# Performance work log

Hardware: AMD Instinct MI355X
Metric: run time of the kernel (lower is better)

The kernel has to match this reference:

```python
import jax, jax.numpy as jnp
import numpy as np

N, IN_DIM, D, H, L, E, MAX_DEG = 50000, 128, 128, 16, 3, 800000, 512
C = D // H  # head dim


def _ln(x, scale, bias, eps=1e-5):
    mu = x.mean(-1, keepdims=True)
    var = ((x - mu) ** 2).mean(-1, keepdims=True)
    return (x - mu) * jax.lax.rsqrt(var + eps) * scale + bias


def setup_inputs() -> dict:
    key = jax.random.key(0)
    ks = jax.random.split(key, 20)
    s = 0.02
    inp = {
        "x": jax.random.normal(ks[0], (N, IN_DIM), jnp.float32),
        "edge_index": jax.random.randint(ks[1], (2, E), 0, N, jnp.int32),
        "W_in": jax.random.normal(ks[2], (IN_DIM, D), jnp.float32) * s,
        "b_in": jnp.zeros((D,), jnp.float32),
        "in_emb": jax.random.normal(ks[3], (MAX_DEG + 1, D), jnp.float32) * s,
        "out_emb": jax.random.normal(ks[4], (MAX_DEG + 1, D), jnp.float32) * s,
        "ln_scale": jnp.ones((L, D), jnp.float32),
        "ln_bias": jnp.zeros((L, D), jnp.float32),
        "Wq": jax.random.normal(ks[5], (L, D, D), jnp.float32) * s,
        "bq": jnp.zeros((L, D), jnp.float32),
        "Wk": jax.random.normal(ks[6], (L, D, D), jnp.float32) * s,
        "bk": jnp.zeros((L, D), jnp.float32),
        "Wv": jax.random.normal(ks[7], (L, D, D), jnp.float32) * s,
        "bv": jnp.zeros((L, D), jnp.float32),
        "Wskip": jax.random.normal(ks[8], (L, D, D), jnp.float32) * s,
        "bskip": jnp.zeros((L, D), jnp.float32),
        "Wbeta": jax.random.normal(ks[9], (L, 3 * D, 1), jnp.float32) * s,
        "fn_scale": jnp.ones((D,), jnp.float32),
        "fn_bias": jnp.zeros((D,), jnp.float32),
    }
    return inp


def _transformer_conv(h, src, tgt, Wq, bq, Wk, bk, Wv, bv, Wskip, bskip, Wbeta):
    # PyG TransformerConv, beta=True, concat=True, eval mode (no dropout)
    q = (h @ Wq + bq).reshape(N, H, C)
    k = (h @ Wk + bk).reshape(N, H, C)
    v = (h @ Wv + bv).reshape(N, H, C)
    # per-edge attention logits [E, H]
    alpha = (q[tgt] * k[src]).sum(-1) / jnp.sqrt(jnp.float32(C))
    # scatter-softmax over incoming edges of each target node
    m = jax.ops.segment_max(alpha, tgt, num_segments=N)
    ex = jnp.exp(alpha - m[tgt])
    den = jax.ops.segment_sum(ex, tgt, num_segments=N)
    w = ex / den[tgt]  # [E, H]
    msg = v[src] * w[:, :, None]  # [E, H, C]
    out = jax.ops.segment_sum(msg, tgt, num_segments=N).reshape(N, D)
    # root skip + gated beta combination
    xr = h @ Wskip + bskip
    beta = jax.nn.sigmoid(jnp.concatenate([out, xr, out - xr], axis=-1) @ Wbeta)
    return beta * xr + (1.0 - beta) * out


def reference(x, edge_index, W_in, b_in, in_emb, out_emb, ln_scale, ln_bias,
              Wq, bq, Wk, bk, Wv, bv, Wskip, bskip, Wbeta, fn_scale, fn_bias):
    src, tgt = edge_index[0], edge_index[1]
    h = x @ W_in + b_in
    # centrality encoding: in/out degree embeddings
    ones = jnp.ones((E,), jnp.float32)
    idg = jnp.clip(jax.ops.segment_sum(ones, tgt, num_segments=N), 0, MAX_DEG).astype(jnp.int32)
    odg = jnp.clip(jax.ops.segment_sum(ones, src, num_segments=N), 0, MAX_DEG).astype(jnp.int32)
    h = h + in_emb[idg] + out_emb[odg]
    for l in range(L):
        hn = _ln(h, ln_scale[l], ln_bias[l])
        h = h + _transformer_conv(hn, src, tgt, Wq[l], bq[l], Wk[l], bk[l],
                                  Wv[l], bv[l], Wskip[l], bskip[l], Wbeta[l])
    return _ln(h, fn_scale, fn_bias)
```

## Files before the change

kernel.cpp:

```cpp
#include <hip/hip_runtime.h>
#include <math.h>
#include <stdint.h>

#define NN 50000
#define DM 128
#define NH 16
#define HC 8
#define NL 3
#define NE 800000
#define MAXDEG 512
#define NRG 1563

#define NB2 782
#define NBLK 256
#define CNTN (NB2 * NBLK)
#define SC1 196
#define RNG 4
#define REP 16

typedef __attribute__((ext_vector_type(8))) short short8;
typedef __attribute__((ext_vector_type(4))) float f32x4;
typedef __attribute__((ext_vector_type(2))) float f32x2;

static __device__ __forceinline__ unsigned short f2bf(float x) {
    union { float f; unsigned int u; } v; v.f = x;
    unsigned int r = (v.u + 0x7fffu + ((v.u >> 16) & 1u)) >> 16;
    return (unsigned short)r;
}
static __device__ __forceinline__ float bf2f(unsigned short b) {
    union { unsigned int u; float f; } v; v.u = ((unsigned int)b) << 16;
    return v.f;
}

__global__ __launch_bounds__(1024) void hist_out_kernel(const int* __restrict__ ei,
                                                        unsigned int* __restrict__ part) {
    __shared__ unsigned int hp[8192];
    int rg = blockIdx.x;
    int rp = blockIdx.y;
    int t = threadIdx.x;
    for (int i = t; i < 8192; i += 1024) hp[i] = 0;
    __syncthreads();
    int lo = rg << 14;
    for (int e = rp * 1024 + t; e < NE; e += REP * 1024) {
        int s = ei[e] - lo;
        if ((unsigned)s < 16384u)
            atomicAdd(&hp[s >> 1], (s & 1) ? 0x10000u : 1u);
    }
    __syncthreads();
    unsigned int* pp = part + (size_t)(rg * REP + rp) * 8192;
    for (int i = t; i < 8192; i += 1024) pp[i] = hp[i];
}
__global__ __launch_bounds__(256) void hist_reduce_kernel(const unsigned int* __restrict__ part,
                                                          int* __restrict__ outdeg) {
    int wd = blockIdx.x * 256 + threadIdx.x;
    if (wd >= 25000) return;
    int rg = wd >> 13, lw = wd & 8191;
    unsigned int sum = 0;
#pragma unroll
    for (int r = 0; r < REP; r++)
        sum += part[(size_t)(rg * REP + r) * 8192 + lw];
    outdeg[2 * wd] = sum & 0xffff;
    if (2 * wd + 1 < NN) outdeg[2 * wd + 1] = sum >> 16;
}

__global__ __launch_bounds__(256) void p1_count_kernel(const int* __restrict__ ei,
                                                       int* __restrict__ cnt) {
    __shared__ int hh[NB2];
    int t = threadIdx.x, blk = blockIdx.x;
    for (int b = t; b < NB2; b += 256) hh[b] = 0;
    __syncthreads();
    for (int e = blk * 256 + t; e < NE; e += NBLK * 256)
        atomicAdd(&hh[ei[NE + e] >> 6], 1);
    __syncthreads();
    for (int b = t; b < NB2; b += 256) cnt[b * NBLK + blk] = hh[b];
}

__global__ __launch_bounds__(1024) void gscan1_kernel(int* __restrict__ data,
                                                      int* __restrict__ bsum, int n) {
    __shared__ int sd[1024];
    int t = threadIdx.x;
    int i = blockIdx.x * 1024 + t;
    int val = (i < n) ? data[i] : 0;
    sd[t] = val;
    __syncthreads();
    for (int d = 1; d < 1024; d <<= 1) {
        int x = (t >= d) ? sd[t - d] : 0;
        __syncthreads();
        sd[t] += x;
        __syncthreads();
    }
    if (i < n) data[i] = sd[t] - val;
    if (t == 1023) bsum[blockIdx.x] = sd[1023];
}
__global__ void gscan2_kernel(const int* __restrict__ bsum, int* __restrict__ bpre, int nb) {
    int run = 0;
    for (int i = 0; i < nb; i++) { bpre[i] = run; run += bsum[i]; }
}
__global__ __launch_bounds__(1024) void gscan3_kernel(int* __restrict__ data,
                                                      const int* __restrict__ bpre, int n) {
    int i = blockIdx.x * 1024 + threadIdx.x;
    if (i < n) data[i] += bpre[blockIdx.x];
}

__global__ __launch_bounds__(256) void p3_scatter_kernel(const int* __restrict__ ei,
                                                         const int* __restrict__ cnt,
                                                         int* __restrict__ tmp) {
    __shared__ int hh[NB2];
    int t = threadIdx.x, blk = blockIdx.x;
    for (int b = t; b < NB2; b += 256) hh[b] = cnt[b * NBLK + blk];
    __syncthreads();
    for (int e = blk * 256 + t; e < NE; e += NBLK * 256) {
        int s = ei[e], tg = ei[NE + e];
        int pos = atomicAdd(&hh[tg >> 6], 1);
        tmp[pos] = ((tg & 63) << 16) | s;
    }
}

__global__ __launch_bounds__(256) void p4_fine_kernel(const int* __restrict__ tmp,
                                                      const int* __restrict__ cnt,
                                                      int* __restrict__ off,
                                                      int* __restrict__ indeg,
                                                      int* __restrict__ srcs) {
    __shared__ int c64[64], x64[64], cur[64];
    int b = blockIdx.x, t = threadIdx.x;
    int e0 = cnt[b * NBLK];
    int e1 = (b == NB2 - 1) ? NE : cnt[(b + 1) * NBLK];
    if (t < 64) c64[t] = 0;
    __syncthreads();
    for (int i = e0 + t; i < e1; i += 256) atomicAdd(&c64[(tmp[i] >> 16) & 63], 1);
    __syncthreads();
    if (t == 0) {
        int run = 0;
        for (int j = 0; j < 64; j++) { x64[j] = run; cur[j] = e0 + run; run += c64[j]; }
    }
    __syncthreads();
    if (t < 64) {
        int node = b * 64 + t;
        if (node <= NN) off[node] = e0 + x64[t];
        if (node < NN) indeg[node] = c64[t];
    }
    __syncthreads();
    for (int i = e0 + t; i < e1; i += 256) {
        int w = tmp[i];
        int pos = atomicAdd(&cur[(w >> 16) & 63], 1);
        srcs[pos] = w & 0xffff;
    }
}

__global__ __launch_bounds__(256) void wprep_kernel(const float* __restrict__ Wq,
                                                    const float* __restrict__ Wk,
                                                    const float* __restrict__ Wv,
                                                    const float* __restrict__ Ws,
                                                    const float* __restrict__ Win,
                                                    unsigned short* __restrict__ Wt) {
    __shared__ unsigned short lds[128 * 130];
    int bid = blockIdx.x;
    const float* W;
    if (bid == 12) {
        W = Win;
    } else {
        int l = bid >> 2, m = bid & 3;
        W = (m == 0 ? Wq : m == 1 ? Wk : m == 2 ? Wv : Ws) + (size_t)l * DM * DM;
    }
    unsigned short* out = Wt + (size_t)bid * DM * DM;
    int t = threadIdx.x;
    for (int i = t; i < DM * DM; i += 256) {
        int kk = i >> 7, c = i & 127;
        lds[kk * 130 + c] = f2bf(W[i]);
    }
    __syncthreads();
    for (int o = t; o < DM * DM; o += 256) {
        int c = o >> 7, kk = o & 127;
        out[o] = lds[kk * 130 + c];
    }
}

__global__ __launch_bounds__(256) void xcast_kernel(const float* __restrict__ x,
                                                    unsigned short* __restrict__ xb) {
    int i = blockIdx.x * 256 + threadIdx.x;
    float4 xv = ((const float4*)x)[i];
    ushort4 o;
    o.x = f2bf(xv.x); o.y = f2bf(xv.y); o.z = f2bf(xv.z); o.w = f2bf(xv.w);
    ((ushort4*)xb)[i] = o;
}

__global__ __launch_bounds__(256) void gemm_in_mfma(const unsigned short* __restrict__ xb,
                                                    const unsigned short* __restrict__ Wt,
                                                    const float* __restrict__ b,
                                                    const float* __restrict__ in_emb,
                                                    const float* __restrict__ out_emb,
                                                    const int* __restrict__ indeg,
                                                    const int* __restrict__ outdeg,
                                                    float* __restrict__ h) {
    int w = threadIdx.x >> 6;
    int l = threadIdx.x & 63;
    int lr = l & 15, lc = l >> 4;
    int colbase = (w & 1) * 64;
    int rhalf = w >> 1;

    short8 bfrag[4][4];
#pragma unroll
    for (int ct = 0; ct < 4; ct++) {
        const unsigned short* bp = Wt + (size_t)(colbase + ct * 16 + lr) * DM;
#pragma unroll
        for (int kk = 0; kk < 4; kk++)
            bfrag[ct][kk] = *(const short8*)(bp + kk * 32 + lc * 8);
    }

    for (int rg = blockIdx.x * 2 + rhalf; rg < NRG; rg += gridDim.x * 2) {
        int n0 = rg * 32;
        short8 afrag[2][4];
#pragma unroll
        for (int rt = 0; rt < 2; rt++) {
            int row = n0 + rt * 16 + lr;
            if (row >= NN) row = NN - 1;
            const unsigned short* ap = xb + (size_t)row * DM;
#pragma unroll
            for (int kk = 0; kk < 4; kk++)
                afrag[rt][kk] = *(const short8*)(ap + kk * 32 + lc * 8);
        }
        f32x4 acc[2][4];
#pragma unroll
        for (int rt = 0; rt < 2; rt++)
#pragma unroll
            for (int ct = 0; ct < 4; ct++)
                acc[rt][ct] = (f32x4){0.f, 0.f, 0.f, 0.f};
#pragma unroll
        for (int kk = 0; kk < 4; kk++)
#pragma unroll
            for (int rt = 0; rt < 2; rt++)
#pragma unroll
                for (int ct = 0; ct < 4; ct++)
                    acc[rt][ct] = __builtin_amdgcn_mfma_f32_16x16x32_bf16(
                        afrag[rt][kk], bfrag[ct][kk], acc[rt][ct], 0, 0, 0);
#pragma unroll
        for (int rt = 0; rt < 2; rt++) {
#pragma unroll
            for (int j = 0; j < 4; j++) {
                int row = n0 + rt * 16 + lc * 4 + j;
                if (row < NN) {
                    int id = min(indeg[row], MAXDEG);
                    int od = min(outdeg[row], MAXDEG);
#pragma unroll
                    for (int ct = 0; ct < 4; ct++) {
                        int cc = colbase + ct * 16 + lr;
                        h[(size_t)row * DM + cc] = acc[rt][ct][j] + b[cc]
                            + in_emb[id * DM + cc] + out_emb[od * DM + cc];
                    }
                }
            }
        }
    }
}

static __device__ __forceinline__ void ln_body(const float* __restrict__ hp,
                                               const float* __restrict__ sc,
                                               const float* __restrict__ bi,
                                               int lane, float* o0, float* o1) {
    float v0 = hp[lane], v1 = hp[lane + 64];
    float s = v0 + v1;
#pragma unroll
    for (int d = 32; d; d >>= 1) s += __shfl_xor(s, d);
    float mu = s * (1.f / 128.f);
    float d0 = v0 - mu, d1 = v1 - mu;
    float vs = d0 * d0 + d1 * d1;
#pragma unroll
    for (int d = 32; d; d >>= 1) vs += __shfl_xor(vs, d);
    float rstd = rsqrtf(vs * (1.f / 128.f) + 1e-5f);
    *o0 = d0 * rstd * sc[lane] + bi[lane];
    *o1 = d1 * rstd * sc[lane + 64] + bi[lane + 64];
}

__global__ __launch_bounds__(256) void ln_bf16_kernel(const float* __restrict__ h,
                                                      const float* __restrict__ sc,
                                                      const float* __restrict__ bi,
                                                      unsigned short* __restrict__ o) {
    int row = blockIdx.x * 4 + (threadIdx.x >> 6);
    int lane = threadIdx.x & 63;
    float a, b;
    ln_body(h + (size_t)row * DM, sc, bi, lane, &a, &b);
    unsigned short* op = o + (size_t)row * DM;
    op[lane] = f2bf(a);
    op[lane + 64] = f2bf(b);
}

__global__ __launch_bounds__(256) void ln_f32_kernel(const float* __restrict__ h,
                                                     const float* __restrict__ sc,
                                                     const float* __restrict__ bi,
                                                     float* __restrict__ o) {
    int row = blockIdx.x * 4 + (threadIdx.x >> 6);
    int lane = threadIdx.x & 63;
    float a, b;
    ln_body(h + (size_t)row * DM, sc, bi, lane, &a, &b);
    float* op = o + (size_t)row * DM;
    op[lane] = a;
    op[lane + 64] = b;
}

__global__ __launch_bounds__(512) void gemm_qkvs_mfma(const unsigned short* __restrict__ hn,
                                                      const unsigned short* __restrict__ Wt,
                                                      const float* __restrict__ bq, const float* __restrict__ bk,
                                                      const float* __restrict__ bv, const float* __restrict__ bs,
                                                      unsigned short* __restrict__ q,
                                                      unsigned char* __restrict__ kv8,
                                                      unsigned short* __restrict__ xrb) {
    int w = threadIdx.x >> 6;
    int l = threadIdx.x & 63;
    int lr = l & 15, lc = l >> 4;
    int colbase = w * 64;
    int m = w >> 1;
    int cmbase = (w & 1) * 64;

    const float* bptr = (m == 0 ? bq : m == 1 ? bk : m == 2 ? bv : bs);
    short8 bfrag[4][4];
    float biasv[4];
#pragma unroll
    for (int ct = 0; ct < 4; ct++) {
        int col = colbase + ct * 16 + lr;
        const unsigned short* bp = Wt + (size_t)col * DM;
#pragma unroll
        for (int kk = 0; kk < 4; kk++)
            bfrag[ct][kk] = *(const short8*)(bp + kk * 32 + lc * 8);
        biasv[ct] = bptr[cmbase + ct * 16 + lr];
    }

    for (int rg = blockIdx.x; rg < NRG; rg += gridDim.x) {
        int n0 = rg * 32;
        short8 afrag[2][4];
#pragma unroll
        for (int rt = 0; rt < 2; rt++) {
            int row = n0 + rt * 16 + lr;
            if (row >= NN) row = NN - 1;
            const unsigned short* ap = hn + (size_t)row * DM;
#pragma unroll
            for (int kk = 0; kk < 4; kk++)
                afrag[rt][kk] = *(const short8*)(ap + kk * 32 + lc * 8);
        }
        f32x4 acc[2][4];
#pragma unroll
        for (int rt = 0; rt < 2; rt++)
#pragma unroll
            for (int ct = 0; ct < 4; ct++)
                acc[rt][ct] = (f32x4){0.f, 0.f, 0.f, 0.f};
#pragma unroll
        for (int kk = 0; kk < 4; kk++)
#pragma unroll
            for (int rt = 0; rt < 2; rt++)
#pragma unroll
                for (int ct = 0; ct < 4; ct++)
                    acc[rt][ct] = __builtin_amdgcn_mfma_f32_16x16x32_bf16(
                        afrag[rt][kk], bfrag[ct][kk], acc[rt][ct], 0, 0, 0);

        if (m == 0 || m == 3) {
            unsigned short* dst = (m == 0) ? q : xrb;
#pragma unroll
            for (int rt = 0; rt < 2; rt++)
#pragma unroll
                for (int ct = 0; ct < 4; ct++) {
                    int cc = cmbase + ct * 16 + lr;
                    float bb = biasv[ct];
#pragma unroll
                    for (int j = 0; j < 4; j++) {
                        int row = n0 + rt * 16 + lc * 4 + j;
                        if (row < NN) dst[(size_t)row * DM + cc] = f2bf(acc[rt][ct][j] + bb);
                    }
                }
        } else {
            unsigned char* base = kv8 + ((m == 1) ? 0 : 4);
#pragma unroll
            for (int rt = 0; rt < 2; rt++)
#pragma unroll
                for (int ct = 0; ct < 4; ct++) {
                    int cc = cmbase + ct * 16 + lr;
                    int goff = (cc >> 2) * 8;
                    float bb = biasv[ct];
#pragma unroll
                    for (int j = 0; j < 4; j++) {
                        float val = acc[rt][ct][j] + bb;
                        float nb = __shfl_xor(val, 1);
                        float a = (lr & 1) ? nb : val;
                        float b2 = (lr & 1) ? val : nb;
                        int w2 = __builtin_amdgcn_cvt_pk_fp8_f32(a, b2, 0, false);
                        int p = __shfl_xor(w2, 2);
                        unsigned int word = (lr & 2)
                            ? ((unsigned int)(p & 0xffff) | ((unsigned int)w2 << 16))
                            : ((unsigned int)(w2 & 0xffff) | ((unsigned int)p << 16));
                        int row = n0 + rt * 16 + lc * 4 + j;
                        if ((lr & 3) == 0 && row < NN)
                            *(unsigned int*)(base + (size_t)row * 256 + goff) = word;
                    }
                }
        }
    }
}

__global__ __launch_bounds__(256) void attn_fused_kernel(const int* __restrict__ off,
                                                         const int* __restrict__ srcs,
                                                         const unsigned short* __restrict__ q,
                                                         const unsigned char* __restrict__ kv8,
                                                         const unsigned short* __restrict__ xrb,
                                                         const float* __restrict__ Wb,
                                                         float* __restrict__ h,
                                                         const float* __restrict__ nsc,
                                                         const float* __restrict__ nbi,
                                                         unsigned short* __restrict__ hn_out) {
    int wv = threadIdx.x >> 6;
    int L = threadIdx.x & 63;
    int half = L >> 5, L5 = L & 31;
    int n = blockIdx.x * 4 + wv;
    int o0 = off[n], o1 = off[n + 1];
    int c4 = L5 * 4;
    const float isq = 0.35355339059f;

    ushort4 qu = *(const ushort4*)(q + (size_t)n * DM + c4);
    float q0 = bf2f(qu.x) * isq, q1 = bf2f(qu.y) * isq,
          q2 = bf2f(qu.z) * isq, q3 = bf2f(qu.w) * isq;

    float den = 0.f, a0 = 0.f, a1 = 0.f, a2 = 0.f, a3 = 0.f;
    for (int p = o0; p < o1; p += 16) {
        int sj[8];
#pragma unroll
        for (int j = 0; j < 8; j++) {
            int e = p + 2 * j + half;
            sj[j] = (e < o1) ? srcs[e] : 0;
        }
        uint2 uu[8];
#pragma unroll
        for (int j = 0; j < 8; j++)
            uu[j] = *(const uint2*)(kv8 + (size_t)sj[j] * 256 + L5 * 8);
#pragma unroll
        for (int j = 0; j < 8; j++) {
            int e = p + 2 * j + half;
            f32x2 k01 = __builtin_amdgcn_cvt_pk_f32_fp8(uu[j].x, false);
            f32x2 k23 = __builtin_amdgcn_cvt_pk_f32_fp8(uu[j].x, true);
            f32x2 v01 = __builtin_amdgcn_cvt_pk_f32_fp8(uu[j].y, false);
            f32x2 v23 = __builtin_amdgcn_cvt_pk_f32_fp8(uu[j].y, true);
            float d = q0 * k01.x + q1 * k01.y + q2 * k23.x + q3 * k23.y;
            d += __shfl_xor(d, 1);
            float e2 = (e < o1) ? __expf(d) : 0.f;
            den += e2;
            a0 += e2 * v01.x;
            a1 += e2 * v01.y;
            a2 += e2 * v23.x;
            a3 += e2 * v23.y;
        }
    }
    den += __shfl_xor(den, 32);
    a0 += __shfl_xor(a0, 32);
    a1 += __shfl_xor(a1, 32);
    a2 += __shfl_xor(a2, 32);
    a3 += __shfl_xor(a3, 32);

    float inv = (den > 0.f) ? 1.f / den : 0.f;
    float o0v = a0 * inv, o1v = a1 * inv, o2v = a2 * inv, o3v = a3 * inv;

    ushort4 xu = *(const ushort4*)(xrb + (size_t)n * DM + c4);
    float x0 = bf2f(xu.x), x1 = bf2f(xu.y), x2 = bf2f(xu.z), x3 = bf2f(xu.w);
    float c = o0v * Wb[c4] + o1v * Wb[c4 + 1] + o2v * Wb[c4 + 2] + o3v * Wb[c4 + 3]
            + x0 * Wb[DM + c4] + x1 * Wb[DM + c4 + 1]
            + x2 * Wb[DM + c4 + 2] + x3 * Wb[DM + c4 + 3]
            + (o0v - x0) * Wb[2 * DM + c4] + (o1v - x1) * Wb[2 * DM + c4 + 1]
            + (o2v - x2) * Wb[2 * DM + c4 + 2] + (o3v - x3) * Wb[2 * DM + c4 + 3];
    if (half) c = 0.f;
#pragma unroll
    for (int d2 = 32; d2; d2 >>= 1) c += __shfl_xor(c, d2);
    float beta = 1.f / (1.f + __expf(-c));

    size_t idx = (size_t)n * DM + c4;
    float4 hv = *(const float4*)(h + idx);
    hv.x += beta * x0 + (1.f - beta) * o0v;
    hv.y += beta * x1 + (1.f - beta) * o1v;
    hv.z += beta * x2 + (1.f - beta) * o2v;
    hv.w += beta * x3 + (1.f - beta) * o3v;
    if (half == 0) *(float4*)(h + idx) = hv;

    if (hn_out) {
        float s = hv.x + hv.y + hv.z + hv.w;
#pragma unroll
        for (int d2 = 16; d2; d2 >>= 1) s += __shfl_xor(s, d2);
        float mu = s * (1.f / 128.f);
        float d0 = hv.x - mu, d1 = hv.y - mu, d2_ = hv.z - mu, d3 = hv.w - mu;
        float vs = d0 * d0 + d1 * d1 + d2_ * d2_ + d3 * d3;
#pragma unroll
        for (int d2 = 16; d2; d2 >>= 1) vs += __shfl_xor(vs, d2);
        float rstd = rsqrtf(vs * (1.f / 128.f) + 1e-5f);
        float4 scv = *(const float4*)(nsc + c4);
        float4 biv = *(const float4*)(nbi + c4);
        ushort4 o;
        o.x = f2bf(d0 * rstd * scv.x + biv.x);
        o.y = f2bf(d1 * rstd * scv.y + biv.y);
        o.z = f2bf(d2_ * rstd * scv.z + biv.z);
        o.w = f2bf(d3 * rstd * scv.w + biv.w);
        if (half == 0) *(ushort4*)(hn_out + idx) = o;
    }
}

static inline char* alignup(char* p) {
    return (char*)(((uintptr_t)p + 255) & ~(uintptr_t)255);
}

extern "C" void kernel_launch(void* const* d_in, const int* in_sizes, int n_in,
                              void* d_out, int out_size, void* d_ws, size_t ws_size,
                              hipStream_t stream) {
    const float* x       = (const float*)d_in[0];
    const int*   ei      = (const int*)d_in[1];
    const float* W_in    = (const float*)d_in[2];
    const float* b_in    = (const float*)d_in[3];
    const float* in_emb  = (const float*)d_in[4];
    const float* out_emb = (const float*)d_in[5];
    const float* ln_sc   = (const float*)d_in[6];
    const float* ln_bi   = (const float*)d_in[7];
    const float* Wq      = (const float*)d_in[8];
    const float* bq      = (const float*)d_in[9];
    const float* Wk      = (const float*)d_in[10];
    const float* bk      = (const float*)d_in[11];
    const float* Wv      = (const float*)d_in[12];
    const float* bv      = (const float*)d_in[13];
    const float* Wsk     = (const float*)d_in[14];
    const float* bsk     = (const float*)d_in[15];
    const float* Wbeta   = (const float*)d_in[16];
    const float* fn_sc   = (const float*)d_in[17];
    const float* fn_bi   = (const float*)d_in[18];

    char* w = (char*)d_ws;
    int* indeg  = (int*)w; w = alignup(w + (size_t)NN * 4);
    int* outdeg = (int*)w; w = alignup(w + (size_t)NN * 4);
    int* off    = (int*)w; w = alignup(w + (size_t)(NN + 1) * 4);
    int* srcs   = (int*)w; w = alignup(w + (size_t)NE * 4);
    int* tmp    = (int*)w; w = alignup(w + (size_t)NE * 4);
    int* cnt    = (int*)w; w = alignup(w + (size_t)CNTN * 4);
    int* bsum   = (int*)w; w = alignup(w + (size_t)SC1 * 4);
    int* bpre   = (int*)w; w = alignup(w + (size_t)SC1 * 4);
    unsigned int* hpart = (unsigned int*)w; w = alignup(w + (size_t)RNG * REP * 8192 * 4);
    float* h    = (float*)w; w = alignup(w + (size_t)NN * DM * 4);
    unsigned short* hn  = (unsigned short*)w; w = alignup(w + (size_t)NN * DM * 2);
    unsigned short* q   = (unsigned short*)w; w = alignup(w + (size_t)NN * DM * 2);
    unsigned short* xrb = (unsigned short*)w; w = alignup(w + (size_t)NN * DM * 2);
    unsigned char*  kv8 = (unsigned char*)w;  w = alignup(w + (size_t)NN * 256);
    unsigned short* xb  = (unsigned short*)w; w = alignup(w + (size_t)NN * DM * 2);
    unsigned short* Wt  = (unsigned short*)w; w = alignup(w + (size_t)13 * DM * DM * 2);

    hist_out_kernel<<<dim3(RNG, REP), 1024, 0, stream>>>(ei, hpart);
    hist_reduce_kernel<<<98, 256, 0, stream>>>(hpart, outdeg);
    p1_count_kernel<<<NBLK, 256, 0, stream>>>(ei, cnt);
    gscan1_kernel<<<SC1, 1024, 0, stream>>>(cnt, bsum, CNTN);
    gscan2_kernel<<<1, 1, 0, stream>>>(bsum, bpre, SC1);
    gscan3_kernel<<<SC1, 1024, 0, stream>>>(cnt, bpre, CNTN);
    p3_scatter_kernel<<<NBLK, 256, 0, stream>>>(ei, cnt, tmp);
    p4_fine_kernel<<<NB2, 256, 0, stream>>>(tmp, cnt, off, indeg, srcs);

    wprep_kernel<<<13, 256, 0, stream>>>(Wq, Wk, Wv, Wsk, W_in, Wt);
    xcast_kernel<<<NN * DM / 4 / 256, 256, 0, stream>>>(x, xb);

    gemm_in_mfma<<<391, 256, 0, stream>>>(xb, Wt + (size_t)12 * DM * DM, b_in,
                                          in_emb, out_emb, indeg, outdeg, h);
    ln_bf16_kernel<<<NN / 4, 256, 0, stream>>>(h, ln_sc, ln_bi, hn);
    for (int l = 0; l < NL; l++) {
        gemm_qkvs_mfma<<<391, 512, 0, stream>>>(hn,
            Wt + (size_t)l * 4 * DM * DM,
            bq + l * DM, bk + l * DM, bv + l * DM, bsk + l * DM,
            q, kv8, xrb);
        bool last = (l == NL - 1);
        attn_fused_kernel<<<NN / 4, 256, 0, stream>>>(off, srcs, q, kv8, xrb,
            Wbeta + (size_t)l * 3 * DM, h,
            last ? (const float*)nullptr : ln_sc + (l + 1) * DM,
            last ? (const float*)nullptr : ln_bi + (l + 1) * DM,
            last ? (unsigned short*)nullptr : hn);
    }
    ln_f32_kernel<<<NN / 4, 256, 0, stream>>>(h, fn_sc, fn_bi, (float*)d_out);
}
```

Measured before the change: 387.8 us.

## Stage QKV/skip GEMM outputs through swizzled LDS for coalesced vector stores

The QKV+skip GEMM writes its bias-added bf16 results into a swizzled shared-memory tile instead of scattering 2-byte stores straight from MFMA fragments. After a barrier, each thread writes 16-byte coalesced rows of q and xr, and packs k/v into interleaved fp8 words. The grid now launches one block per 32-row group instead of a persistent loop, so weight fragments are reloaded per block. k and v are rounded to bf16 before the fp8 conversion, which adds a double rounding step.

```diff
diff --git a/kernel.cpp b/kernel.cpp
--- a/kernel.cpp
+++ b/kernel.cpp
@@ -304,6 +304,8 @@
                                                       unsigned short* __restrict__ q,
                                                       unsigned char* __restrict__ kv8,
                                                       unsigned short* __restrict__ xrb) {
+    __shared__ unsigned short qlds[8 * 2048];
+
     int w = threadIdx.x >> 6;
     int l = threadIdx.x & 63;
     int lr = l & 15, lc = l >> 4;
@@ -324,73 +326,82 @@
         biasv[ct] = bptr[cmbase + ct * 16 + lr];
     }
 
-    for (int rg = blockIdx.x; rg < NRG; rg += gridDim.x) {
-        int n0 = rg * 32;
-        short8 afrag[2][4];
-#pragma unroll
-        for (int rt = 0; rt < 2; rt++) {
-            int row = n0 + rt * 16 + lr;
-            if (row >= NN) row = NN - 1;
-            const unsigned short* ap = hn + (size_t)row * DM;
-#pragma unroll
-            for (int kk = 0; kk < 4; kk++)
-                afrag[rt][kk] = *(const short8*)(ap + kk * 32 + lc * 8);
+    int n0 = blockIdx.x * 32;
+    short8 afrag[2][4];
+#pragma unroll
+    for (int rt = 0; rt < 2; rt++) {
+        int row = n0 + rt * 16 + lr;
+        if (row >= NN) row = NN - 1;
+        const unsigned short* ap = hn + (size_t)row * DM;
+#pragma unroll
+        for (int kk = 0; kk < 4; kk++)
+            afrag[rt][kk] = *(const short8*)(ap + kk * 32 + lc * 8);
+    }
+    f32x4 acc[2][4];
+#pragma unroll
+    for (int rt = 0; rt < 2; rt++)
+#pragma unroll
+        for (int ct = 0; ct < 4; ct++)
+            acc[rt][ct] = (f32x4){0.f, 0.f, 0.f, 0.f};
+#pragma unroll
+    for (int kk = 0; kk < 4; kk++)
+#pragma unroll
+        for (int rt = 0; rt < 2; rt++)
+#pragma unroll
+            for (int ct = 0; ct < 4; ct++)
+                acc[rt][ct] = __builtin_amdgcn_mfma_f32_16x16x32_bf16(
+                    afrag[rt][kk], bfrag[ct][kk], acc[rt][ct], 0, 0, 0);
+
+    unsigned short* tile = qlds + w * 2048;
+#pragma unroll
+    for (int rt = 0; rt < 2; rt++)
+#pragma unroll
+        for (int ct = 0; ct < 4; ct++) {
+            float bb = biasv[ct];
+            int grp = ct ^ lc;
+#pragma unroll
+            for (int j = 0; j < 4; j++) {
+                int rloc = rt * 16 + lc * 4 + j;
+                tile[rloc * 64 + grp * 16 + lr] = f2bf(acc[rt][ct][j] + bb);
+            }
         }
-        f32x4 acc[2][4];
-#pragma unroll
-        for (int rt = 0; rt < 2; rt++)
-#pragma unroll
-            for (int ct = 0; ct < 4; ct++)
-                acc[rt][ct] = (f32x4){0.f, 0.f, 0.f, 0.f};
-#pragma unroll
-        for (int kk = 0; kk < 4; kk++)
-#pragma unroll
-            for (int rt = 0; rt < 2; rt++)
-#pragma unroll
-                for (int ct = 0; ct < 4; ct++)
-                    acc[rt][ct] = __builtin_amdgcn_mfma_f32_16x16x32_bf16(
-                        afrag[rt][kk], bfrag[ct][kk], acc[rt][ct], 0, 0, 0);
-
-        if (m == 0 || m == 3) {
-            unsigned short* dst = (m == 0) ? q : xrb;
-#pragma unroll
-            for (int rt = 0; rt < 2; rt++)
-#pragma unroll
-                for (int ct = 0; ct < 4; ct++) {
-                    int cc = cmbase + ct * 16 + lr;
-                    float bb = biasv[ct];
-#pragma unroll
-                    for (int j = 0; j < 4; j++) {
-                        int row = n0 + rt * 16 + lc * 4 + j;
-                        if (row < NN) dst[(size_t)row * DM + cc] = f2bf(acc[rt][ct][j] + bb);
-                    }
-                }
-        } else {
-            unsigned char* base = kv8 + ((m == 1) ? 0 : 4);
-#pragma unroll
-            for (int rt = 0; rt < 2; rt++)
-#pragma unroll
-                for (int ct = 0; ct < 4; ct++) {
-                    int cc = cmbase + ct * 16 + lr;
-                    int goff = (cc >> 2) * 8;
-                    float bb = biasv[ct];
-#pragma unroll
-                    for (int j = 0; j < 4; j++) {
-                        float val = acc[rt][ct][j] + bb;
-                        float nb = __shfl_xor(val, 1);
-                        float a = (lr & 1) ? nb : val;
-                        float b2 = (lr & 1) ? val : nb;
-                        int w2 = __builtin_amdgcn_cvt_pk_fp8_f32(a, b2, 0, false);
-                        int p = __shfl_xor(w2, 2);
-                        unsigned int word = (lr & 2)
-                            ? ((unsigned int)(p & 0xffff) | ((unsigned int)w2 << 16))
-                            : ((unsigned int)(w2 & 0xffff) | ((unsigned int)p << 16));
-                        int row = n0 + rt * 16 + lc * 4 + j;
-                        if ((lr & 3) == 0 && row < NN)
-                            *(unsigned int*)(base + (size_t)row * 256 + goff) = word;
-                    }
-                }
+    __syncthreads();
+
+    int t5 = threadIdx.x;
+    int r = t5 >> 4;
+    int g = t5 & 15;
+    int row = n0 + r;
+    if (row < NN) {
+        int c0 = g * 8;
+        int c0L = c0 & 63;
+        int sw = (r >> 2) & 3;
+        int loff = r * 64 + (((c0L >> 4) ^ sw) << 4) + (c0L & 15);
+        int hi = c0 >> 6;
+
+        short8 vq = *(const short8*)(qlds + (0 * 2 + hi) * 2048 + loff);
+        *(short8*)(q + (size_t)row * DM + c0) = vq;
+        short8 vx = *(const short8*)(qlds + (3 * 2 + hi) * 2048 + loff);
+        *(short8*)(xrb + (size_t)row * DM + c0) = vx;
+        short8 vk = *(const short8*)(qlds + (1 * 2 + hi) * 2048 + loff);
+        short8 vv = *(const short8*)(qlds + (2 * 2 + hi) * 2048 + loff);
+        float kf[8], vf[8];
+#pragma unroll
+        for (int i = 0; i < 8; i++) {
+            kf[i] = bf2f((unsigned short)vk[i]);
+            vf[i] = bf2f((unsigned short)vv[i]);
         }
+        int w0 = __builtin_amdgcn_cvt_pk_fp8_f32(kf[0], kf[1], 0, false);
+        w0 = __builtin_amdgcn_cvt_pk_fp8_f32(kf[2], kf[3], w0, true);
+        int w1 = __builtin_amdgcn_cvt_pk_fp8_f32(vf[0], vf[1], 0, false);
+        w1 = __builtin_amdgcn_cvt_pk_fp8_f32(vf[2], vf[3], w1, true);
+        int w2 = __builtin_amdgcn_cvt_pk_fp8_f32(kf[4], kf[5], 0, false);
+        w2 = __builtin_amdgcn_cvt_pk_fp8_f32(kf[6], kf[7], w2, true);
+        int w3 = __builtin_amdgcn_cvt_pk_fp8_f32(vf[4], vf[5], 0, false);
+        w3 = __builtin_amdgcn_cvt_pk_fp8_f32(vf[6], vf[7], w3, true);
+        uint4 st;
+        st.x = (unsigned int)w0; st.y = (unsigned int)w1;
+        st.z = (unsigned int)w2; st.w = (unsigned int)w3;
+        *(uint4*)(kv8 + (size_t)row * 256 + g * 16) = st;
     }
 }
 
@@ -556,7 +567,7 @@
                                           in_emb, out_emb, indeg, outdeg, h);
     ln_bf16_kernel<<<NN / 4, 256, 0, stream>>>(h, ln_sc, ln_bi, hn);
     for (int l = 0; l < NL; l++) {
-        gemm_qkvs_mfma<<<391, 512, 0, stream>>>(hn,
+        gemm_qkvs_mfma<<<NRG, 512, 0, stream>>>(hn,
             Wt + (size_t)l * 4 * DM * DM,
             bq + l * DM, bk + l * DM, bv + l * DM, bsk + l * DM,
             q, kv8, xrb);
```

After: 404.1 us. 4.2% more time.
